# Kernel tuning notes

Hardware: AMD Instinct MI355X
Metric: run time of the kernel (lower is better)

The kernel has to match this reference:

```python
import jax, jax.numpy as jnp
import numpy as np

B, L, C = 4, 2052, 1024
H, D = 16, 64          # num_heads, head_dim
NREG = 4               # register tokens, bypass RoPE
LN_EPS = 1e-5


def setup_inputs() -> dict:
    key = jax.random.key(0)
    ks = jax.random.split(key, 6)
    s = 1.0 / np.sqrt(C)
    return {
        "x": jax.random.normal(ks[0], (B, L, C), jnp.float32),
        "rope_embed": jax.random.normal(ks[1], (2, L - NREG, D), jnp.float32),  # [cos; sin]
        "Wqkv": jax.random.normal(ks[2], (C, 3 * C), jnp.float32) * s,
        "bqkv": jnp.zeros((3 * C,), jnp.float32),
        "Wproj": jax.random.normal(ks[3], (C, C), jnp.float32) * s,
        "bproj": jnp.zeros((C,), jnp.float32),
        "ln_gamma": jnp.ones((C,), jnp.float32),
        "ln_beta": jnp.zeros((C,), jnp.float32),
    }


def _rotate_half(x):
    x1, x2 = jnp.split(x, 2, axis=-1)
    return jnp.concatenate([-x2, x1], axis=-1)


def _apply_rope(q, k, rope_embed, n_reg):
    # q,k: (B,H,L,D); rope_embed: (2, L-n_reg, D)
    cos = rope_embed[0][None, None]  # (1,1,Ls,D)
    sin = rope_embed[1][None, None]
    def rot(t):
        reg, sp = t[:, :, :n_reg], t[:, :, n_reg:]
        sp = sp * cos + _rotate_half(sp) * sin
        return jnp.concatenate([reg, sp], axis=2)
    return rot(q), rot(k)


def reference(x, rope_embed, Wqkv, bqkv, Wproj, bproj, ln_gamma, ln_beta):
    # QKV projection: (B,L,3C) -> (3,B,H,L,D)
    qkv = (x @ Wqkv + bqkv).reshape(B, L, 3, H, D).transpose(2, 0, 3, 1, 4)
    q, k, v = qkv[0], qkv[1], qkv[2]
    q, k = _apply_rope(q, k, rope_embed, NREG)
    # SDPA (no dropout, not causal)
    scale = 1.0 / np.sqrt(D)
    logits = jnp.einsum("bhqd,bhkd->bhqk", q, k) * scale
    attn = jax.nn.softmax(logits, axis=-1)
    out = jnp.einsum("bhqk,bhkd->bhqd", attn, v)
    out = out.transpose(0, 2, 1, 3).reshape(B, L, C)
    # post-attention LayerNorm
    mu = jnp.mean(out, axis=-1, keepdims=True)
    var = jnp.mean(jnp.square(out - mu), axis=-1, keepdims=True)
    out = (out - mu) * jax.lax.rsqrt(var + LN_EPS) * ln_gamma + ln_beta
    # output projection
    return out @ Wproj + bproj
```

## Files before the change

### kernel.cpp

```cpp
#include <hip/hip_runtime.h>
#include <hip/hip_bf16.h>

#define B_ 4
#define L_ 2052
#define C_ 1024
#define H_ 16
#define D_ 64
#define NREG_ 4
#define M_ (B_*L_)
#define LP_ 2056
#define QSC 0.18033688f

typedef short bf16x8 __attribute__((ext_vector_type(8)));
typedef float f32x4 __attribute__((ext_vector_type(4)));
typedef __hip_bfloat16 bf16;

#define MFMA(a,b,c) __builtin_amdgcn_mfma_f32_16x16x32_bf16(a,b,c,0,0,0)

__device__ inline float b2f(bf16 v){ return __bfloat162float(v); }
__device__ inline bf16  f2b(float v){ return __float2bfloat16(v); }

__global__ __launch_bounds__(256)
void cvt_split(const float* __restrict__ in, bf16* __restrict__ hi,
               bf16* __restrict__ lo, int n)
{
    int i = (blockIdx.x*256 + threadIdx.x)*4;
    if (i >= n) return;
    float4 v = *(const float4*)(in + i);
    int2 hraw, lraw;
    bf16* hp = (bf16*)&hraw;
    bf16* lp = (bf16*)&lraw;
    float vv[4] = {v.x, v.y, v.z, v.w};
    #pragma unroll
    for (int j=0;j<4;++j){
        bf16 h = f2b(vv[j]);
        hp[j] = h;
        lp[j] = f2b(vv[j] - b2f(h));
    }
    *(int2*)(hi + i) = hraw;
    *(int2*)(lo + i) = lraw;
}

__global__ __launch_bounds__(256)
void transpose_cvt(const float* __restrict__ in, bf16* __restrict__ out,
                   int R, int Cc)
{
    __shared__ bf16 t[32][33];
    int bx = blockIdx.x * 32;
    int by = blockIdx.y * 32;
    int tx = threadIdx.x;
    int ty = threadIdx.y;
    #pragma unroll
    for (int i=0;i<4;++i){
        int r = by + ty + i*8;
        int c = bx + tx;
        t[ty+i*8][tx] = f2b(in[(size_t)r*Cc + c]);
    }
    __syncthreads();
    #pragma unroll
    for (int i=0;i<4;++i){
        int r = bx + ty + i*8;
        int c = by + tx;
        out[(size_t)r*R + c] = t[tx][ty+i*8];
    }
}

template<typename OutT, bool SPLIT>
__global__ __launch_bounds__(256,2)
void gemm_wide(const bf16* __restrict__ A, const bf16* __restrict__ Alo,
               const bf16* __restrict__ Bt, const float* __restrict__ bias,
               OutT* __restrict__ C, int M, int N, int K)
{
    __shared__ bf16 As[128*40];
    __shared__ bf16 Als[SPLIT ? 128*40 : 8];
    __shared__ bf16 Bs[256*40];

    int tid  = threadIdx.x;
    int lane = tid & 63, wave = tid >> 6;
    int wm = (wave>>1)*64, wn = (wave&1)*128;
    int bm = blockIdx.y*128, bn = blockIdx.x*256;
    int lrow = lane & 15, lk8 = (lane>>4)*8;
    int quad = lane >> 4;

    f32x4 acc[4][8] = {};

    int r0 = tid >> 2;
    int c0 = (tid & 3) * 8;

    for (int k0 = 0; k0 < K; k0 += 32) {
        #pragma unroll
        for (int it=0; it<2; ++it) {
            int r = r0 + it*64;
            int ga = bm + r;
            int4 va = {0,0,0,0}, vl = {0,0,0,0};
            if (ga < M) {
                va = *(const int4*)(A + (size_t)ga*K + k0 + c0);
                if constexpr (SPLIT)
                    vl = *(const int4*)(Alo + (size_t)ga*K + k0 + c0);
            }
            *(int4*)(&As[r*40 + c0]) = va;
            if constexpr (SPLIT) *(int4*)(&Als[r*40 + c0]) = vl;
        }
        #pragma unroll
        for (int it=0; it<4; ++it) {
            int r = r0 + it*64;
            int4 vb = *(const int4*)(Bt + (size_t)(bn + r)*K + k0 + c0);
            *(int4*)(&Bs[r*40 + c0]) = vb;
        }
        __syncthreads();

        bf16x8 b[8];
        #pragma unroll
        for (int i=0;i<8;++i)
            b[i] = *(const bf16x8*)(&Bs[(wn+i*16+lrow)*40 + lk8]);
        #pragma unroll
        for (int mi=0;mi<4;++mi){
            bf16x8 a = *(const bf16x8*)(&As[(wm+mi*16+lrow)*40 + lk8]);
            #pragma unroll
            for (int ni=0;ni<8;++ni)
                acc[mi][ni] = MFMA(a, b[ni], acc[mi][ni]);
            if constexpr (SPLIT) {
                bf16x8 al = *(const bf16x8*)(&Als[(wm+mi*16+lrow)*40 + lk8]);
                #pragma unroll
                for (int ni=0;ni<8;++ni)
                    acc[mi][ni] = MFMA(al, b[ni], acc[mi][ni]);
            }
        }
        __syncthreads();
    }

    #pragma unroll
    for (int ni=0;ni<8;++ni){
        int col = bn + wn + ni*16 + lrow;
        float bv = bias[col];
        #pragma unroll
        for (int mi=0;mi<4;++mi){
            int rowb = bm + wm + mi*16 + quad*4;
            #pragma unroll
            for (int r=0;r<4;++r){
                int row = rowb + r;
                if (row < M) {
                    float v = acc[mi][ni][r] + bv;
                    if constexpr (sizeof(OutT)==4) C[(size_t)row*N + col] = v;
                    else                           C[(size_t)row*N + col] = f2b(v);
                }
            }
        }
    }
}

__global__ __launch_bounds__(256)
void rope_kernel(bf16* __restrict__ qkv, const float* __restrict__ rope)
{
    int idx = blockIdx.x*256 + threadIdx.x;
    int d = idx & 31;
    int h = (idx >> 5) & 15;
    int m = idx >> 9;
    if (m >= M_) return;
    int l = m % L_;
    if (l < NREG_) return;
    const float* cp = rope + (size_t)(l - NREG_)*D_;
    const float* sp = rope + (size_t)(L_ - NREG_)*D_ + (size_t)(l - NREG_)*D_;
    float c0 = cp[d], c1 = cp[d+32], s0 = sp[d], s1 = sp[d+32];
    size_t base = (size_t)m*3072 + h*64;
    {
        float a = b2f(qkv[base + d]), b = b2f(qkv[base + d + 32]);
        qkv[base + d]      = f2b(a*c0 - b*s0);
        qkv[base + d + 32] = f2b(b*c1 + a*s1);
    }
    {
        size_t kb = base + 1024;
        float a = b2f(qkv[kb + d]), b = b2f(qkv[kb + d + 32]);
        qkv[kb + d]      = f2b(a*c0 - b*s0);
        qkv[kb + d + 32] = f2b(b*c1 + a*s1);
    }
}

__global__ __launch_bounds__(256)
void transpose_v(const bf16* __restrict__ qkv, bf16* __restrict__ Vt)
{
    __shared__ bf16 t[64*72];
    int bh = blockIdx.y, lt = blockIdx.x;
    int b = bh >> 4, h = bh & 15;
    int tid = threadIdx.x;
    #pragma unroll
    for (int it=0; it<2; ++it){
        int i = tid + it*256;
        int il = i >> 3, c = (i&7)*8;
        int l = lt*64 + il;
        int4 v = {0,0,0,0};
        if (l < L_) v = *(const int4*)(qkv + ((size_t)b*L_ + l)*3072 + 2048 + h*64 + c);
        *(int4*)(&t[il*72 + c]) = v;
    }
    __syncthreads();
    #pragma unroll
    for (int it=0; it<2; ++it){
        int i = tid + it*256;
        int d = i >> 3, ck = (i&7)*8;
        if (lt*64 + ck + 8 <= LP_){
            union { int4 q; bf16 e[8]; } u;
            #pragma unroll
            for (int j=0;j<8;++j) u.e[j] = t[(ck+j)*72 + d];
            *(int4*)(&Vt[((size_t)bh*64 + d)*LP_ + lt*64 + ck]) = u.q;
        }
    }
}

__global__ __launch_bounds__(256)
void attn_kernel(const bf16* __restrict__ qkv, const bf16* __restrict__ Vt,
                 float* __restrict__ out)
{
    __shared__ bf16 sQP[10752];
    __shared__ bf16 sK[64*72];
    __shared__ bf16 sV[64*72];

    int tid = threadIdx.x, lane = tid & 63, wave = tid >> 6;
    int lrow = lane & 15, lk8 = (lane>>4)*8, quad = lane >> 4;
    int qt = blockIdx.x, bh = blockIdx.y;
    int b  = bh >> 4, h = bh & 15;
    size_t rowbase = (size_t)b * L_;
    int q0 = qt * 128;

    #pragma unroll
    for (int it=0; it<4; ++it){
        int i = tid + it*256;
        int r = i >> 3;
        int c = (i & 7) * 8;
        int lq = q0 + r;
        int4 v = {0,0,0,0};
        if (lq < L_) v = *(const int4*)(qkv + (rowbase + lq)*3072 + h*64 + c);
        *(int4*)(&sQP[r*72 + c]) = v;
    }
    __syncthreads();

    bf16x8 qf[2][2];
    #pragma unroll
    for (int qi=0;qi<2;++qi)
        #pragma unroll
        for (int s=0;s<2;++s)
            qf[qi][s] = *(const bf16x8*)(&sQP[(wave*32 + qi*16 + lrow)*72 + s*32 + lk8]);

    float lst[2] = {0.f, 0.f};
    f32x4 o_[2][4] = {};

    bf16* pw = &sQP[wave*2688];
    const int nkt = (L_ + 63) / 64;

    int4 kr[2], vr[2];
    {
        #pragma unroll
        for (int it=0; it<2; ++it){
            int i = tid + it*256;
            int r = i >> 3, c = (i & 7)*8;
            int lk = r;
            kr[it] = (lk < L_) ? *(const int4*)(qkv + (rowbase+lk)*3072 + 1024 + h*64 + c)
                               : (int4){0,0,0,0};
            vr[it] = *(const int4*)(Vt + ((size_t)bh*64 + r)*LP_ + c);
        }
    }

    for (int kt = 0; kt < nkt; ++kt) {
        __syncthreads();
        #pragma unroll
        for (int it=0; it<2; ++it){
            int i = tid + it*256;
            int r = i >> 3, c = (i & 7)*8;
            *(int4*)(&sK[r*72 + c]) = kr[it];
            *(int4*)(&sV[r*72 + c]) = vr[it];
        }
        __syncthreads();
        if (kt+1 < nkt){
            #pragma unroll
            for (int it=0; it<2; ++it){
                int i = tid + it*256;
                int r = i >> 3, c = (i & 7)*8;
                int lk = (kt+1)*64 + r;
                kr[it] = (lk < L_) ? *(const int4*)(qkv + (rowbase+lk)*3072 + 1024 + h*64 + c)
                                   : (int4){0,0,0,0};
                int vc = (kt+1)*64 + c;
                vr[it] = (vc + 8 <= LP_) ? *(const int4*)(Vt + ((size_t)bh*64 + r)*LP_ + vc)
                                         : (int4){0,0,0,0};
            }
        }

        bool full = (kt != 32);
        {
            bf16x8 kf[4][2];
            #pragma unroll
            for (int ki=0;ki<4;++ki)
                #pragma unroll
                for (int s=0;s<2;++s)
                    kf[ki][s] = *(const bf16x8*)(&sK[(ki*16+lrow)*72 + s*32 + lk8]);
            #pragma unroll
            for (int ki=0;ki<4;++ki){
                #pragma unroll
                for (int qi=0;qi<2;++qi){
                    f32x4 t = {};
                    t = MFMA(kf[ki][0], qf[qi][0], t);
                    t = MFMA(kf[ki][1], qf[qi][1], t);
                    float p[4];
                    #pragma unroll
                    for (int r=0;r<4;++r){
                        float e = __builtin_amdgcn_exp2f(t[r]*QSC);
                        p[r] = (full || (2048 + ki*16 + quad*4 + r) < L_) ? e : 0.f;
                        lst[qi] += p[r];
                    }
                    union { int2 d2; __hip_bfloat162 h2[2]; } u;
                    u.h2[0] = __float22bfloat162_rn({p[0], p[1]});
                    u.h2[1] = __float22bfloat162_rn({p[2], p[3]});
                    *(int2*)(&pw[(qi*16 + lrow)*72 + ki*16 + quad*4]) = u.d2;
                }
            }
        }

        bf16x8 vf[4][2];
        #pragma unroll
        for (int ni=0;ni<4;++ni)
            #pragma unroll
            for (int s=0;s<2;++s)
                vf[ni][s] = *(const bf16x8*)(&sV[(ni*16+lrow)*72 + s*32 + lk8]);
        bf16x8 pf[2][2];
        #pragma unroll
        for (int mi=0;mi<2;++mi)
            #pragma unroll
            for (int s=0;s<2;++s)
                pf[mi][s] = *(const bf16x8*)(&pw[(mi*16 + lrow)*72 + s*32 + quad*8]);
        #pragma unroll
        for (int mi=0;mi<2;++mi)
            #pragma unroll
            for (int ni=0;ni<4;++ni){
                f32x4 t = o_[mi][ni];
                t = MFMA(pf[mi][0], vf[ni][0], t);
                t = MFMA(pf[mi][1], vf[ni][1], t);
                o_[mi][ni] = t;
            }
    }

    #pragma unroll
    for (int qi=0;qi<2;++qi){
        lst[qi] += __shfl_xor(lst[qi], 16);
        lst[qi] += __shfl_xor(lst[qi], 32);
    }

    #pragma unroll
    for (int mi=0;mi<2;++mi)
        #pragma unroll
        for (int r=0;r<4;++r){
            float sum = __shfl(lst[mi], quad*4 + r);
            float inv = 1.f / sum;
            int lq = q0 + wave*32 + mi*16 + quad*4 + r;
            if (lq < L_){
                size_t base = (rowbase + lq)*1024 + h*64;
                #pragma unroll
                for (int ni=0;ni<4;++ni)
                    out[base + ni*16 + lrow] = o_[mi][ni][r]*inv;
            }
        }
}

__global__ __launch_bounds__(256)
void ln_kernel(const float* __restrict__ in, const float* __restrict__ gamma,
               const float* __restrict__ beta, bf16* __restrict__ y)
{
    int row = blockIdx.x;
    int tid = threadIdx.x;
    int wave = tid >> 6, lane = tid & 63;
    float4 v4 = *(const float4*)(in + (size_t)row*1024 + tid*4);
    float v[4] = {v4.x, v4.y, v4.z, v4.w};
    float s = 0.f, q = 0.f;
    #pragma unroll
    for (int j=0;j<4;++j){ s += v[j]; q += v[j]*v[j]; }
    #pragma unroll
    for (int o=1;o<64;o<<=1){ s += __shfl_xor(s, o); q += __shfl_xor(q, o); }
    __shared__ float sh[8];
    if (lane == 0){ sh[wave] = s; sh[4+wave] = q; }
    __syncthreads();
    s = sh[0]+sh[1]+sh[2]+sh[3];
    q = sh[4]+sh[5]+sh[6]+sh[7];
    float mu  = s * (1.f/1024.f);
    float var = q * (1.f/1024.f) - mu*mu;
    float rstd = rsqrtf(var + 1e-5f);
    int2 raw;
    bf16* ob = (bf16*)&raw;
    #pragma unroll
    for (int j=0;j<4;++j){
        float g = gamma[tid*4+j], be = beta[tid*4+j];
        ob[j] = f2b((v[j]-mu)*rstd*g + be);
    }
    *(int2*)(y + (size_t)row*1024 + tid*4) = raw;
}

extern "C" void kernel_launch(void* const* d_in, const int* in_sizes, int n_in,
                              void* d_out, int out_size, void* d_ws, size_t ws_size,
                              hipStream_t stream)
{
    const float* x     = (const float*)d_in[0];
    const float* rope  = (const float*)d_in[1];
    const float* Wqkv  = (const float*)d_in[2];
    const float* bqkv  = (const float*)d_in[3];
    const float* Wproj = (const float*)d_in[4];
    const float* bproj = (const float*)d_in[5];
    const float* lng   = (const float*)d_in[6];
    const float* lnb   = (const float*)d_in[7];
    float* out = (float*)d_out;

    char* ws = (char*)d_ws;
    size_t off = 0;
    auto alloc = [&](size_t bytes)->char* {
        char* p = ws + off;
        off += (bytes + 255) & ~(size_t)255;
        return p;
    };
    bf16* xhi    = (bf16*)alloc((size_t)M_*C_*2);
    bf16* xlo    = (bf16*)alloc((size_t)M_*C_*2);
    bf16* WqkvT  = (bf16*)alloc((size_t)3*C_*C_*2);
    bf16* WprojT = (bf16*)alloc((size_t)C_*C_*2);
    bf16* qkv    = (bf16*)alloc((size_t)M_*3*C_*2);
    bf16* Vt     = (bf16*)alloc((size_t)B_*H_*D_*LP_*2);

    float* attnF = (float*)xhi;
    bf16*  y     = qkv;

    cvt_split<<<M_*C_/1024, 256, 0, stream>>>(x, xhi, xlo, M_*C_);
    transpose_cvt<<<dim3(3*C_/32, C_/32), dim3(32,8), 0, stream>>>(Wqkv, WqkvT, C_, 3*C_);
    transpose_cvt<<<dim3(C_/32, C_/32), dim3(32,8), 0, stream>>>(Wproj, WprojT, C_, C_);
    gemm_wide<bf16, true><<<dim3(3*C_/256, (M_+127)/128), 256, 0, stream>>>(
        xhi, xlo, WqkvT, bqkv, qkv, M_, 3*C_, C_);
    rope_kernel<<<(M_*H_*32)/256, 256, 0, stream>>>(qkv, rope);
    transpose_v<<<dim3((L_+63)/64, B_*H_), 256, 0, stream>>>(qkv, Vt);
    attn_kernel<<<dim3((L_+127)/128, B_*H_), 256, 0, stream>>>(qkv, Vt, attnF);
    ln_kernel<<<M_, 256, 0, stream>>>(attnF, lng, lnb, y);
    gemm_wide<float, false><<<dim3(C_/256, (M_+127)/128), 256, 0, stream>>>(
        y, nullptr, WprojT, bproj, out, M_, C_, C_);
}
```

Measured before the change: 473.7 us.

## Keep softmax probabilities in registers via permuted K rows, MFMA row sums

The attention kernel loads K rows in a permuted order so that the exp'd score fragments produced by the QK^T MFMA already match the operand layout needed for the PV MFMA. This removes the LDS round-trip of the P tile and its associated reads. The softmax denominator is now accumulated with an extra MFMA against a ones vector instead of per-lane adds and shuffles. The output is transposed so each lane writes float4 vectors. The trade-off is extra MFMA work for row sums and more index arithmetic in the key mask; the first-tile load also drops its bounds check.

```diff
diff --git a/kernel.cpp b/kernel.cpp
--- a/kernel.cpp
+++ b/kernel.cpp
@@ -19,6 +19,7 @@
 
 __device__ inline float b2f(bf16 v){ return __bfloat162float(v); }
 __device__ inline bf16  f2b(float v){ return __float2bfloat16(v); }
+__device__ inline bf16x8 as8(int4 v){ union{int4 i; bf16x8 b;} u; u.i=v; return u.b; }
 
 __global__ __launch_bounds__(256)
 void cvt_split(const float* __restrict__ in, bf16* __restrict__ hi,
@@ -210,7 +211,7 @@
 void attn_kernel(const bf16* __restrict__ qkv, const bf16* __restrict__ Vt,
                  float* __restrict__ out)
 {
-    __shared__ bf16 sQP[10752];
+    __shared__ bf16 sQ[128*72];
     __shared__ bf16 sK[64*72];
     __shared__ bf16 sV[64*72];
 
@@ -229,7 +230,7 @@
         int lq = q0 + r;
         int4 v = {0,0,0,0};
         if (lq < L_) v = *(const int4*)(qkv + (rowbase + lq)*3072 + h*64 + c);
-        *(int4*)(&sQP[r*72 + c]) = v;
+        *(int4*)(&sQ[r*72 + c]) = v;
     }
     __syncthreads();
 
@@ -238,12 +239,15 @@
     for (int qi=0;qi<2;++qi)
         #pragma unroll
         for (int s=0;s<2;++s)
-            qf[qi][s] = *(const bf16x8*)(&sQP[(wave*32 + qi*16 + lrow)*72 + s*32 + lk8]);
-
-    float lst[2] = {0.f, 0.f};
+            qf[qi][s] = *(const bf16x8*)(&sQ[(wave*32 + qi*16 + lrow)*72 + s*32 + lk8]);
+
     f32x4 o_[2][4] = {};
-
-    bf16* pw = &sQP[wave*2688];
+    f32x4 lsum[2] = {};
+
+    bf16x8 onesf;
+    #pragma unroll
+    for (int j=0;j<8;++j) onesf[j] = (short)0x3F80;
+
     const int nkt = (L_ + 63) / 64;
 
     int4 kr[2], vr[2];
@@ -252,9 +256,8 @@
         for (int it=0; it<2; ++it){
             int i = tid + it*256;
             int r = i >> 3, c = (i & 7)*8;
-            int lk = r;
-            kr[it] = (lk < L_) ? *(const int4*)(qkv + (rowbase+lk)*3072 + 1024 + h*64 + c)
-                               : (int4){0,0,0,0};
+            int pr = (r & 0x23) | ((r & 0x0C) << 1) | ((r & 0x10) >> 2);
+            kr[it] = *(const int4*)(qkv + (rowbase + pr)*3072 + 1024 + h*64 + c);
             vr[it] = *(const int4*)(Vt + ((size_t)bh*64 + r)*LP_ + c);
         }
     }
@@ -274,7 +277,8 @@
             for (int it=0; it<2; ++it){
                 int i = tid + it*256;
                 int r = i >> 3, c = (i & 7)*8;
-                int lk = (kt+1)*64 + r;
+                int pr = (r & 0x23) | ((r & 0x0C) << 1) | ((r & 0x10) >> 2);
+                int lk = (kt+1)*64 + pr;
                 kr[it] = (lk < L_) ? *(const int4*)(qkv + (rowbase+lk)*3072 + 1024 + h*64 + c)
                                    : (int4){0,0,0,0};
                 int vc = (kt+1)*64 + c;
@@ -284,78 +288,65 @@
         }
 
         bool full = (kt != 32);
-        {
-            bf16x8 kf[4][2];
-            #pragma unroll
-            for (int ki=0;ki<4;++ki)
+        int4 pb[2][2];
+
+        #pragma unroll
+        for (int ki=0; ki<4; ++ki){
+            bf16x8 kf0 = *(const bf16x8*)(&sK[(ki*16+lrow)*72 + lk8]);
+            bf16x8 kf1 = *(const bf16x8*)(&sK[(ki*16+lrow)*72 + 32 + lk8]);
+            #pragma unroll
+            for (int qi=0; qi<2; ++qi){
+                f32x4 t = {};
+                t = MFMA(kf0, qf[qi][0], t);
+                t = MFMA(kf1, qf[qi][1], t);
+                float p[4];
                 #pragma unroll
-                for (int s=0;s<2;++s)
-                    kf[ki][s] = *(const bf16x8*)(&sK[(ki*16+lrow)*72 + s*32 + lk8]);
-            #pragma unroll
-            for (int ki=0;ki<4;++ki){
-                #pragma unroll
-                for (int qi=0;qi<2;++qi){
-                    f32x4 t = {};
-                    t = MFMA(kf[ki][0], qf[qi][0], t);
-                    t = MFMA(kf[ki][1], qf[qi][1], t);
-                    float p[4];
-                    #pragma unroll
-                    for (int r=0;r<4;++r){
-                        float e = __builtin_amdgcn_exp2f(t[r]*QSC);
-                        p[r] = (full || (2048 + ki*16 + quad*4 + r) < L_) ? e : 0.f;
-                        lst[qi] += p[r];
-                    }
-                    union { int2 d2; __hip_bfloat162 h2[2]; } u;
-                    u.h2[0] = __float22bfloat162_rn({p[0], p[1]});
-                    u.h2[1] = __float22bfloat162_rn({p[2], p[3]});
-                    *(int2*)(&pw[(qi*16 + lrow)*72 + ki*16 + quad*4]) = u.d2;
+                for (int r=0;r<4;++r){
+                    float e = __builtin_amdgcn_exp2f(t[r]*QSC);
+                    int keyi = (ki>>1)*32 + quad*8 + (ki&1)*4 + r;
+                    p[r] = (full || (2048 + keyi) < L_) ? e : 0.f;
                 }
-            }
-        }
-
-        bf16x8 vf[4][2];
-        #pragma unroll
-        for (int ni=0;ni<4;++ni)
-            #pragma unroll
-            for (int s=0;s<2;++s)
-                vf[ni][s] = *(const bf16x8*)(&sV[(ni*16+lrow)*72 + s*32 + lk8]);
-        bf16x8 pf[2][2];
-        #pragma unroll
-        for (int mi=0;mi<2;++mi)
-            #pragma unroll
-            for (int s=0;s<2;++s)
-                pf[mi][s] = *(const bf16x8*)(&pw[(mi*16 + lrow)*72 + s*32 + quad*8]);
-        #pragma unroll
-        for (int mi=0;mi<2;++mi)
-            #pragma unroll
-            for (int ni=0;ni<4;++ni){
+                union { int2 d2; __hip_bfloat162 h2[2]; } u;
+                u.h2[0] = __float22bfloat162_rn({p[0], p[1]});
+                u.h2[1] = __float22bfloat162_rn({p[2], p[3]});
+                if ((ki & 1) == 0){ pb[qi][ki>>1].x = u.d2.x; pb[qi][ki>>1].y = u.d2.y; }
+                else              { pb[qi][ki>>1].z = u.d2.x; pb[qi][ki>>1].w = u.d2.y; }
+            }
+        }
+
+        #pragma unroll
+        for (int ni=0; ni<4; ++ni){
+            bf16x8 vf0 = *(const bf16x8*)(&sV[(ni*16+lrow)*72 + lk8]);
+            bf16x8 vf1 = *(const bf16x8*)(&sV[(ni*16+lrow)*72 + 32 + lk8]);
+            #pragma unroll
+            for (int mi=0; mi<2; ++mi){
                 f32x4 t = o_[mi][ni];
-                t = MFMA(pf[mi][0], vf[ni][0], t);
-                t = MFMA(pf[mi][1], vf[ni][1], t);
+                t = MFMA(vf0, as8(pb[mi][0]), t);
+                t = MFMA(vf1, as8(pb[mi][1]), t);
                 o_[mi][ni] = t;
             }
-    }
-
-    #pragma unroll
-    for (int qi=0;qi<2;++qi){
-        lst[qi] += __shfl_xor(lst[qi], 16);
-        lst[qi] += __shfl_xor(lst[qi], 32);
-    }
-
-    #pragma unroll
-    for (int mi=0;mi<2;++mi)
-        #pragma unroll
-        for (int r=0;r<4;++r){
-            float sum = __shfl(lst[mi], quad*4 + r);
-            float inv = 1.f / sum;
-            int lq = q0 + wave*32 + mi*16 + quad*4 + r;
-            if (lq < L_){
-                size_t base = (rowbase + lq)*1024 + h*64;
-                #pragma unroll
-                for (int ni=0;ni<4;++ni)
-                    out[base + ni*16 + lrow] = o_[mi][ni][r]*inv;
-            }
-        }
+        }
+        #pragma unroll
+        for (int mi=0; mi<2; ++mi){
+            lsum[mi] = MFMA(onesf, as8(pb[mi][0]), lsum[mi]);
+            lsum[mi] = MFMA(onesf, as8(pb[mi][1]), lsum[mi]);
+        }
+    }
+
+    #pragma unroll
+    for (int mi=0; mi<2; ++mi){
+        float inv = 1.f / lsum[mi][0];
+        int lq = q0 + wave*32 + mi*16 + lrow;
+        if (lq < L_){
+            size_t base = (rowbase + lq)*1024 + h*64;
+            #pragma unroll
+            for (int ni=0; ni<4; ++ni){
+                f32x4 t = o_[mi][ni];
+                float4 w = {t[0]*inv, t[1]*inv, t[2]*inv, t[3]*inv};
+                *(float4*)(&out[base + ni*16 + quad*4]) = w;
+            }
+        }
+    }
 }
 
 __global__ __launch_bounds__(256)
```

Result: faster. 448.8 us (-5.3%).
